# Optimization experiments

Measured on AMD Instinct MI355X. Metric: run time of the kernel, lower is better.

The kernel has to match this reference:

```python
import jax, jax.numpy as jnp
import numpy as np

N_NODES = 100000   # total atoms in the batched graph
N_EDGES = 1600000  # bonds (directed), avg degree 16
N_GRAPHS = 2000    # molecules in the batch
D_IN, D_H, D_OUT = 600, 300, 2  # 600 = embedding_dim(150) * 4


def setup_inputs() -> dict:
    key = jax.random.key(0)
    ks = jax.random.split(key, 8)
    node_feats = jax.random.normal(ks[0], (N_NODES, D_IN), dtype=jnp.float32)
    W1 = jax.random.normal(ks[1], (D_IN, D_H), dtype=jnp.float32) * (1.0 / np.sqrt(D_IN))
    b1 = jnp.zeros((D_H,), dtype=jnp.float32)
    W2 = jax.random.normal(ks[2], (D_H, D_H), dtype=jnp.float32) * (1.0 / np.sqrt(D_H))
    b2 = jnp.zeros((D_H,), dtype=jnp.float32)
    Wfc = jax.random.normal(ks[3], (D_H, D_OUT), dtype=jnp.float32) * (1.0 / np.sqrt(D_H))
    bfc = jnp.zeros((D_OUT,), dtype=jnp.float32)
    src = jax.random.randint(ks[4], (N_EDGES,), 0, N_NODES, dtype=jnp.int32).astype(jnp.int64)
    dst = jax.random.randint(ks[5], (N_EDGES,), 0, N_NODES, dtype=jnp.int32).astype(jnp.int64)
    graph_id = jnp.sort(jax.random.randint(ks[6], (N_NODES,), 0, N_GRAPHS, dtype=jnp.int32)).astype(jnp.int64)
    return {"node_feats": node_feats, "W1": W1, "b1": b1, "W2": W2, "b2": b2,
            "Wfc": Wfc, "bfc": bfc, "src": src, "dst": dst, "graph_id": graph_id}


def _gcn_layer(x, W, b, src, dst, inv_sqrt_out, inv_sqrt_in):
    # DGL GraphConv (norm='both'): h_i = d_i^{-1/2} * sum_{j->i} d_j^{-1/2} (x_j W) + b
    # weight applied before aggregation (in_feats >= out_feats path), math identical either way.
    h = x @ W                                  # [N, d_out]
    m = h * inv_sqrt_out[:, None]              # scale by src out-degree^{-1/2}
    agg = jax.ops.segment_sum(m[src], dst, num_segments=N_NODES)  # [N, d_out]
    return agg * inv_sqrt_in[:, None] + b


def reference(node_feats, W1, b1, W2, b2, Wfc, bfc, src, dst, graph_id):
    ones_e = jnp.ones((src.shape[0],), dtype=node_feats.dtype)
    deg_out = jax.ops.segment_sum(ones_e, src, num_segments=N_NODES)
    deg_in = jax.ops.segment_sum(ones_e, dst, num_segments=N_NODES)
    inv_sqrt_out = jnp.where(deg_out > 0, jax.lax.rsqrt(jnp.maximum(deg_out, 1.0)), 0.0)
    inv_sqrt_in = jnp.where(deg_in > 0, jax.lax.rsqrt(jnp.maximum(deg_in, 1.0)), 0.0)

    h = jax.nn.relu(_gcn_layer(node_feats, W1, b1, src, dst, inv_sqrt_out, inv_sqrt_in))
    h = jax.nn.relu(_gcn_layer(h, W2, b2, src, dst, inv_sqrt_out, inv_sqrt_in))
    p = jax.nn.softmax(h @ Wfc + bfc, axis=-1)  # [N, 2] per-node class probs

    # per-graph mean pooling (unbatch + mean over each graph's nodes)
    pooled_sum = jax.ops.segment_sum(p, graph_id, num_segments=N_GRAPHS)
    counts = jax.ops.segment_sum(jnp.ones((N_NODES,), dtype=p.dtype), graph_id, num_segments=N_GRAPHS)
    return pooled_sum / jnp.maximum(counts, 1.0)[:, None]  # [G, 2]
```

## Files before the change

kernel.cpp:

```cpp
#include <hip/hip_runtime.h>
#include <hip/hip_bf16.h>
#include <hip/hip_fp8.h>

#define N_NODES 100000
#define N_EDGES 1600000
#define N_GRAPHS 2000
#define D_IN 600
#define D_H 300
#define D_OUT 2

#define NPAD 320
#define K1PAD 640
#define K2PAD 320
#define MPAD 100096

typedef __bf16 bf16;
typedef __bf16 bf16x8 __attribute__((ext_vector_type(8)));
typedef float f32x4 __attribute__((ext_vector_type(4)));

__device__ __forceinline__ void gload16(const void* g, void* l) {
    __builtin_amdgcn_global_load_lds(
        (const __attribute__((address_space(1))) unsigned int*)g,
        (__attribute__((address_space(3))) unsigned int*)l, 16, 0, 0);
}

__device__ __forceinline__ float f8f(unsigned int b) {
    __hip_fp8_e4m3 t; t.__x = (__hip_fp8_storage_t)b; return (float)t;
}
__device__ __forceinline__ unsigned char ff8(float f) {
    __hip_fp8_e4m3 t(f); return (unsigned char)t.__x;
}

__global__ __launch_bounds__(256) void count_deg(const int* __restrict__ src,
                                                 const int* __restrict__ dst,
                                                 int* __restrict__ deg_out,
                                                 int* __restrict__ deg_in) {
    int e = blockIdx.x * blockDim.x + threadIdx.x;
    if (e < N_EDGES) {
        atomicAdd(&deg_out[src[e]], 1);
        atomicAdd(&deg_in[dst[e]], 1);
    }
}

__global__ __launch_bounds__(256) void block_sum(const int* __restrict__ deg_in,
                                                 int* __restrict__ bsum) {
    __shared__ int s[256];
    int i = blockIdx.x * 256 + threadIdx.x;
    s[threadIdx.x] = (i < N_NODES) ? deg_in[i] : 0;
    __syncthreads();
    for (int off = 128; off; off >>= 1) {
        if (threadIdx.x < off) s[threadIdx.x] += s[threadIdx.x + off];
        __syncthreads();
    }
    if (threadIdx.x == 0) bsum[blockIdx.x] = s[0];
}

__global__ void scan_serial(const int* __restrict__ bsum, int* __restrict__ boff, int nb) {
    if (threadIdx.x == 0 && blockIdx.x == 0) {
        int run = 0;
        for (int i = 0; i < nb; ++i) { boff[i] = run; run += bsum[i]; }
    }
}

__global__ __launch_bounds__(256) void node_offsets(const int* __restrict__ deg_in,
                                                    const int* __restrict__ deg_out,
                                                    const int* __restrict__ boff,
                                                    int* __restrict__ row_start,
                                                    int* __restrict__ cursor,
                                                    float* __restrict__ inv_in,
                                                    float* __restrict__ inv_out) {
    __shared__ int s[256];
    int i = blockIdx.x * 256 + threadIdx.x;
    int d = (i < N_NODES) ? deg_in[i] : 0;
    s[threadIdx.x] = d;
    __syncthreads();
    for (int off = 1; off < 256; off <<= 1) {
        int v = 0;
        if (threadIdx.x >= off) v = s[threadIdx.x - off];
        __syncthreads();
        if (threadIdx.x >= off) s[threadIdx.x] += v;
        __syncthreads();
    }
    if (i < N_NODES) {
        int excl = s[threadIdx.x] - d;
        int rs = boff[blockIdx.x] + excl;
        row_start[i] = rs;
        cursor[i] = rs;
        int di = deg_in[i];
        int dout = deg_out[i];
        inv_in[i]  = (di   > 0) ? rsqrtf((float)di)   : 0.0f;
        inv_out[i] = (dout > 0) ? rsqrtf((float)dout) : 0.0f;
    }
}

__global__ __launch_bounds__(256) void fill_csr(const int* __restrict__ src,
                                                const int* __restrict__ dst,
                                                int* __restrict__ cursor,
                                                int* __restrict__ adj) {
    int e = blockIdx.x * blockDim.x + threadIdx.x;
    if (e < N_EDGES) {
        int pos = atomicAdd(&cursor[dst[e]], 1);
        adj[pos] = src[e];
    }
}

__global__ __launch_bounds__(256) void conv_bt(const float* __restrict__ W, bf16* __restrict__ Bt,
                                               int K, int N, int Kpad) {
    int idx = blockIdx.x * 256 + threadIdx.x;
    int k = idx % Kpad;
    int n = idx / Kpad;
    if (n >= NPAD) return;
    bf16 v = (bf16)0.0f;
    if (k < K && n < N) v = (bf16)W[(size_t)k * N + n];
    Bt[(size_t)n * Kpad + k] = v;
}

__global__ __launch_bounds__(256) void prep_small(const float* __restrict__ b1,
                                                  const float* __restrict__ b2,
                                                  const float* __restrict__ Wfc,
                                                  float* __restrict__ b1p,
                                                  float* __restrict__ b2p,
                                                  float* __restrict__ wfcp) {
    int i = blockIdx.x * 256 + threadIdx.x;
    if (i < NPAD) {
        b1p[i] = (i < D_H) ? b1[i] : 0.f;
        b2p[i] = (i < D_H) ? b2[i] : 0.f;
    }
    if (i < NPAD * 2) {
        wfcp[i] = (i < D_H * 2) ? Wfc[i] : 0.f;
    }
}

__global__ __launch_bounds__(512) void mfma_gemm_f32A(const float* __restrict__ A,
                                                      const bf16* __restrict__ Bt,
                                                      const float* __restrict__ rowscale,
                                                      unsigned char* __restrict__ C8) {
    __shared__ bf16 As[128 * 64];
    __shared__ bf16 Bs[320 * 64];
    const int tid = threadIdx.x;
    const int lane = tid & 63;
    const int wid = tid >> 6;
    const int wr = wid >> 2;
    const int wc = wid & 3;
    const int blockRow = blockIdx.x * 128;
    const size_t rowBytesB = (size_t)K1PAD * 2;

    f32x4 acc[4][5] = {};

    const int nK = K1PAD >> 6;
    for (int t = 0; t < nK; ++t) {
        const size_t kByte = (size_t)t * 128;
#pragma unroll
        for (int c = 0; c < 2; ++c) {
            int o = c * 8192 + tid * 16;
            int row = o >> 7;
            int slot = (o >> 4) & 7;
            int gr = blockRow + row;
            int k = t * 64 + slot * 8;
            bf16x8 v = {};
            if (gr < N_NODES && k < D_IN) {
                const float* p = A + (size_t)gr * D_IN + k;
                float4 f0 = *(const float4*)p;
                float4 f1 = *(const float4*)(p + 4);
                v[0] = (bf16)f0.x; v[1] = (bf16)f0.y; v[2] = (bf16)f0.z; v[3] = (bf16)f0.w;
                v[4] = (bf16)f1.x; v[5] = (bf16)f1.y; v[6] = (bf16)f1.z; v[7] = (bf16)f1.w;
            }
            int waddr = row * 128 + ((slot ^ (row & 7)) << 4);
            *(bf16x8*)((char*)As + waddr) = v;
        }
#pragma unroll
        for (int c = 0; c < 5; ++c) {
            int o = c * 8192 + tid * 16;
            int row = o >> 7;
            int slot = (o >> 4) & 7;
            int srcs = slot ^ (row & 7);
            const char* g = (const char*)Bt + (size_t)row * rowBytesB + kByte + srcs * 16;
            gload16(g, (char*)Bs + o);
        }
        __syncthreads();
#pragma unroll
        for (int kk = 0; kk < 2; ++kk) {
            int slot = kk * 4 + (lane >> 4);
            bf16x8 af[4], bfr[5];
#pragma unroll
            for (int mi = 0; mi < 4; ++mi) {
                int row = wr * 64 + mi * 16 + (lane & 15);
                int addr = row * 128 + ((slot ^ (row & 7)) << 4);
                af[mi] = *(const bf16x8*)((const char*)As + addr);
            }
#pragma unroll
            for (int ni = 0; ni < 5; ++ni) {
                int row = wc * 80 + ni * 16 + (lane & 15);
                int addr = row * 128 + ((slot ^ (row & 7)) << 4);
                bfr[ni] = *(const bf16x8*)((const char*)Bs + addr);
            }
#pragma unroll
            for (int mi = 0; mi < 4; ++mi)
#pragma unroll
                for (int ni = 0; ni < 5; ++ni)
                    acc[mi][ni] = __builtin_amdgcn_mfma_f32_16x16x32_bf16(af[mi], bfr[ni], acc[mi][ni], 0, 0, 0);
        }
        __syncthreads();
    }
#pragma unroll
    for (int mi = 0; mi < 4; ++mi) {
#pragma unroll
        for (int i = 0; i < 4; ++i) {
            int gr = blockRow + wr * 64 + mi * 16 + ((lane >> 4) << 2) + i;
            if (gr >= N_NODES) continue;
            float sc = rowscale[gr];
#pragma unroll
            for (int ni = 0; ni < 5; ++ni) {
                int gc = wc * 80 + ni * 16 + (lane & 15);
                C8[(size_t)gr * NPAD + gc] = ff8(acc[mi][ni][i] * sc);
            }
        }
    }
}

__global__ __launch_bounds__(512) void mfma_gemm(const bf16* __restrict__ A,
                                                 const bf16* __restrict__ Bt,
                                                 const float* __restrict__ rowscale,
                                                 unsigned char* __restrict__ C8,
                                                 int M, int Kpad) {
    __shared__ bf16 As[128 * 64];
    __shared__ bf16 Bs[320 * 64];
    const int tid = threadIdx.x;
    const int lane = tid & 63;
    const int wid = tid >> 6;
    const int wr = wid >> 2;
    const int wc = wid & 3;
    const int blockRow = blockIdx.x * 128;
    const size_t rowBytes = (size_t)Kpad * 2;

    f32x4 acc[4][5] = {};

    const int nK = Kpad >> 6;
    for (int t = 0; t < nK; ++t) {
        const size_t kByte = (size_t)t * 128;
#pragma unroll
        for (int c = 0; c < 2; ++c) {
            int o = c * 8192 + tid * 16;
            int row = o >> 7;
            int slot = (o >> 4) & 7;
            int srcs = slot ^ (row & 7);
            const char* g = (const char*)A + (size_t)(blockRow + row) * rowBytes + kByte + srcs * 16;
            gload16(g, (char*)As + o);
        }
#pragma unroll
        for (int c = 0; c < 5; ++c) {
            int o = c * 8192 + tid * 16;
            int row = o >> 7;
            int slot = (o >> 4) & 7;
            int srcs = slot ^ (row & 7);
            const char* g = (const char*)Bt + (size_t)row * rowBytes + kByte + srcs * 16;
            gload16(g, (char*)Bs + o);
        }
        __syncthreads();
#pragma unroll
        for (int kk = 0; kk < 2; ++kk) {
            int slot = kk * 4 + (lane >> 4);
            bf16x8 af[4], bfr[5];
#pragma unroll
            for (int mi = 0; mi < 4; ++mi) {
                int row = wr * 64 + mi * 16 + (lane & 15);
                int addr = row * 128 + ((slot ^ (row & 7)) << 4);
                af[mi] = *(const bf16x8*)((const char*)As + addr);
            }
#pragma unroll
            for (int ni = 0; ni < 5; ++ni) {
                int row = wc * 80 + ni * 16 + (lane & 15);
                int addr = row * 128 + ((slot ^ (row & 7)) << 4);
                bfr[ni] = *(const bf16x8*)((const char*)Bs + addr);
            }
#pragma unroll
            for (int mi = 0; mi < 4; ++mi)
#pragma unroll
                for (int ni = 0; ni < 5; ++ni)
                    acc[mi][ni] = __builtin_amdgcn_mfma_f32_16x16x32_bf16(af[mi], bfr[ni], acc[mi][ni], 0, 0, 0);
        }
        __syncthreads();
    }
#pragma unroll
    for (int mi = 0; mi < 4; ++mi) {
#pragma unroll
        for (int i = 0; i < 4; ++i) {
            int gr = blockRow + wr * 64 + mi * 16 + ((lane >> 4) << 2) + i;
            if (gr >= M) continue;
            float sc = rowscale[gr];
#pragma unroll
            for (int ni = 0; ni < 5; ++ni) {
                int gc = wc * 80 + ni * 16 + (lane & 15);
                C8[(size_t)gr * NPAD + gc] = ff8(acc[mi][ni][i] * sc);
            }
        }
    }
}

__device__ __forceinline__ void gather_fp8(const unsigned char* __restrict__ m8,
                                           const int* __restrict__ adj,
                                           int s, int d, int lane, float acc[5]) {
    const int cb = lane * 4;
    const int c4 = 256 + lane;
    int e = 0;
    for (; e + 4 <= d; e += 4) {
        const unsigned char* r0 = m8 + (size_t)adj[s + e + 0] * NPAD;
        const unsigned char* r1 = m8 + (size_t)adj[s + e + 1] * NPAD;
        const unsigned char* r2 = m8 + (size_t)adj[s + e + 2] * NPAD;
        const unsigned char* r3 = m8 + (size_t)adj[s + e + 3] * NPAD;
        unsigned int u0 = *(const unsigned int*)(r0 + cb);
        unsigned int u1 = *(const unsigned int*)(r1 + cb);
        unsigned int u2 = *(const unsigned int*)(r2 + cb);
        unsigned int u3 = *(const unsigned int*)(r3 + cb);
        unsigned int b0 = r0[c4], b1 = r1[c4], b2 = r2[c4], b3 = r3[c4];
        acc[0] += (f8f(u0 & 0xff) + f8f(u1 & 0xff)) + (f8f(u2 & 0xff) + f8f(u3 & 0xff));
        acc[1] += (f8f((u0 >> 8) & 0xff) + f8f((u1 >> 8) & 0xff)) + (f8f((u2 >> 8) & 0xff) + f8f((u3 >> 8) & 0xff));
        acc[2] += (f8f((u0 >> 16) & 0xff) + f8f((u1 >> 16) & 0xff)) + (f8f((u2 >> 16) & 0xff) + f8f((u3 >> 16) & 0xff));
        acc[3] += (f8f(u0 >> 24) + f8f(u1 >> 24)) + (f8f(u2 >> 24) + f8f(u3 >> 24));
        acc[4] += (f8f(b0) + f8f(b1)) + (f8f(b2) + f8f(b3));
    }
    for (; e < d; ++e) {
        const unsigned char* r = m8 + (size_t)adj[s + e] * NPAD;
        unsigned int u = *(const unsigned int*)(r + cb);
        acc[0] += f8f(u & 0xff);
        acc[1] += f8f((u >> 8) & 0xff);
        acc[2] += f8f((u >> 16) & 0xff);
        acc[3] += f8f(u >> 24);
        acc[4] += f8f(r[c4]);
    }
}

__global__ __launch_bounds__(256) void aggregate_fp8(const unsigned char* __restrict__ m8,
                                                     const int* __restrict__ row_start,
                                                     const int* __restrict__ deg_in,
                                                     const int* __restrict__ adj,
                                                     const float* __restrict__ inv_in,
                                                     const float* __restrict__ biasp,
                                                     bf16* __restrict__ h) {
    int node = (int)((blockIdx.x * (size_t)blockDim.x + threadIdx.x) >> 6);
    int lane = threadIdx.x & 63;
    if (node >= N_NODES) return;
    int s = row_start[node];
    int d = deg_in[node];
    float acc[5] = {};
    gather_fp8(m8, adj, s, d, lane, acc);
    float sc = inv_in[node];
    int cA = lane * 4;
    int c4 = 256 + lane;
    float4 bq = *(const float4*)(biasp + cA);
    bf16* out = h + (size_t)node * NPAD;
    __bf16 o4[4];
    o4[0] = (bf16)fmaxf(acc[0] * sc + bq.x, 0.f);
    o4[1] = (bf16)fmaxf(acc[1] * sc + bq.y, 0.f);
    o4[2] = (bf16)fmaxf(acc[2] * sc + bq.z, 0.f);
    o4[3] = (bf16)fmaxf(acc[3] * sc + bq.w, 0.f);
    *(float2*)(out + cA) = *(float2*)o4;
    out[c4] = (bf16)fmaxf(acc[4] * sc + biasp[c4], 0.f);
}

__global__ __launch_bounds__(256) void agg2_fc_pool(const unsigned char* __restrict__ m8,
                                                    const int* __restrict__ row_start,
                                                    const int* __restrict__ deg_in,
                                                    const int* __restrict__ adj,
                                                    const float* __restrict__ inv_in,
                                                    const float* __restrict__ biasp,
                                                    const float* __restrict__ wfcp,
                                                    const float* __restrict__ bfc,
                                                    const int* __restrict__ gid,
                                                    float* __restrict__ pooled,
                                                    int* __restrict__ gcount) {
    int node = (int)((blockIdx.x * (size_t)blockDim.x + threadIdx.x) >> 6);
    int lane = threadIdx.x & 63;
    if (node >= N_NODES) return;
    int s = row_start[node];
    int d = deg_in[node];
    float acc[5] = {};
    gather_fp8(m8, adj, s, d, lane, acc);
    float sc = inv_in[node];
    int cA = lane * 4;
    int c4 = 256 + lane;
    float4 bq = *(const float4*)(biasp + cA);
    float h0 = fmaxf(acc[0] * sc + bq.x, 0.f);
    float h1 = fmaxf(acc[1] * sc + bq.y, 0.f);
    float h2 = fmaxf(acc[2] * sc + bq.z, 0.f);
    float h3 = fmaxf(acc[3] * sc + bq.w, 0.f);
    float h4 = fmaxf(acc[4] * sc + biasp[c4], 0.f);
    float4 wA0 = *(const float4*)(wfcp + cA * 2);
    float4 wA1 = *(const float4*)(wfcp + cA * 2 + 4);
    float z0 = h0 * wA0.x + h1 * wA0.z + h2 * wA1.x + h3 * wA1.z;
    float z1 = h0 * wA0.y + h1 * wA0.w + h2 * wA1.y + h3 * wA1.w;
    z0 += h4 * wfcp[c4 * 2];
    z1 += h4 * wfcp[c4 * 2 + 1];
    for (int off = 32; off; off >>= 1) {
        z0 += __shfl_down(z0, off);
        z1 += __shfl_down(z1, off);
    }
    if (lane == 0) {
        float s0 = z0 + bfc[0], s1 = z1 + bfc[1];
        float mx = fmaxf(s0, s1);
        float e0 = __expf(s0 - mx), e1 = __expf(s1 - mx);
        float inv = 1.f / (e0 + e1);
        int g = gid[node];
        atomicAdd(&pooled[g * 2 + 0], e0 * inv);
        atomicAdd(&pooled[g * 2 + 1], e1 * inv);
        atomicAdd(&gcount[g], 1);
    }
}

__global__ __launch_bounds__(256) void finalize(const float* __restrict__ pooled,
                                                const int* __restrict__ gcount,
                                                float* __restrict__ out) {
    int i = blockIdx.x * blockDim.x + threadIdx.x;
    if (i < N_GRAPHS * 2) {
        int g = i >> 1;
        float c = (float)max(gcount[g], 1);
        out[i] = pooled[i] / c;
    }
}

extern "C" void kernel_launch(void* const* d_in, const int* in_sizes, int n_in,
                              void* d_out, int out_size, void* d_ws, size_t ws_size,
                              hipStream_t stream) {
    const float* x   = (const float*)d_in[0];
    const float* W1  = (const float*)d_in[1];
    const float* b1  = (const float*)d_in[2];
    const float* W2  = (const float*)d_in[3];
    const float* b2  = (const float*)d_in[4];
    const float* Wfc = (const float*)d_in[5];
    const float* bfc = (const float*)d_in[6];
    const int* src   = (const int*)d_in[7];
    const int* dst   = (const int*)d_in[8];
    const int* gid   = (const int*)d_in[9];

    char* ws = (char*)d_ws;
    size_t off = 0;
    auto alloc = [&](size_t bytes) -> void* {
        void* p = ws + off;
        off = (off + bytes + 255) & ~(size_t)255;
        return p;
    };
    bf16* h_bf            = (bf16*)alloc((size_t)MPAD * NPAD * 2);
    unsigned char* m8     = (unsigned char*)alloc((size_t)N_NODES * NPAD);
    bf16* B1t    = (bf16*)alloc((size_t)NPAD * K1PAD * 2);
    bf16* B2t    = (bf16*)alloc((size_t)NPAD * K2PAD * 2);
    int*   adj      = (int*)alloc((size_t)N_EDGES * 4);
    int*   row_st   = (int*)alloc((size_t)N_NODES * 4);
    int*   cursor   = (int*)alloc((size_t)N_NODES * 4);
    int*   deg_in   = (int*)alloc((size_t)N_NODES * 4);
    int*   deg_out  = (int*)alloc((size_t)N_NODES * 4);
    float* inv_in   = (float*)alloc((size_t)N_NODES * 4);
    float* inv_out  = (float*)alloc((size_t)N_NODES * 4);
    const int NB = (N_NODES + 255) / 256;
    int*   bsum     = (int*)alloc((size_t)NB * 4);
    int*   boff     = (int*)alloc((size_t)NB * 4);
    float* pooled   = (float*)alloc((size_t)N_GRAPHS * 2 * 4);
    int*   gcount   = (int*)alloc((size_t)N_GRAPHS * 4);
    float* b1p      = (float*)alloc((size_t)NPAD * 4);
    float* b2p      = (float*)alloc((size_t)NPAD * 4);
    float* wfcp     = (float*)alloc((size_t)NPAD * 2 * 4);

    hipMemsetAsync(deg_in, 0, (size_t)N_NODES * 4, stream);
    hipMemsetAsync(deg_out, 0, (size_t)N_NODES * 4, stream);
    hipMemsetAsync(pooled, 0, (size_t)N_GRAPHS * 2 * 4, stream);
    hipMemsetAsync(gcount, 0, (size_t)N_GRAPHS * 4, stream);

    count_deg<<<(N_EDGES + 255) / 256, 256, 0, stream>>>(src, dst, deg_out, deg_in);
    block_sum<<<NB, 256, 0, stream>>>(deg_in, bsum);
    scan_serial<<<1, 64, 0, stream>>>(bsum, boff, NB);
    node_offsets<<<NB, 256, 0, stream>>>(deg_in, deg_out, boff, row_st, cursor, inv_in, inv_out);
    fill_csr<<<(N_EDGES + 255) / 256, 256, 0, stream>>>(src, dst, cursor, adj);

    conv_bt<<<(NPAD * K1PAD + 255) / 256, 256, 0, stream>>>(W1, B1t, D_IN, D_H, K1PAD);
    conv_bt<<<(NPAD * K2PAD + 255) / 256, 256, 0, stream>>>(W2, B2t, D_H, D_H, K2PAD);
    prep_small<<<3, 256, 0, stream>>>(b1, b2, Wfc, b1p, b2p, wfcp);

    mfma_gemm_f32A<<<MPAD / 128, 512, 0, stream>>>(x, B1t, inv_out, m8);
    aggregate_fp8<<<(N_NODES * 64 + 255) / 256, 256, 0, stream>>>(m8, row_st, deg_in, adj, inv_in, b1p, h_bf);
    mfma_gemm<<<MPAD / 128, 512, 0, stream>>>(h_bf, B2t, inv_out, m8, N_NODES, K2PAD);
    agg2_fc_pool<<<(N_NODES * 64 + 255) / 256, 256, 0, stream>>>(m8, row_st, deg_in, adj, inv_in, b2p,
                                                                 wfcp, bfc, gid, pooled, gcount);
    finalize<<<(N_GRAPHS * 2 + 255) / 256, 256, 0, stream>>>(pooled, gcount, (float*)d_out);
}
```

Baseline: 705.9 us.

## Prefetch next GEMM K-tile into registers while computing current tile

Both GEMM kernels are merged into one templated kernel that loads the next K-tile of A and B into registers while the MFMAs of the current tile run, then writes them to LDS after a barrier. This replaces the direct global-to-LDS loads and the synchronous per-tile load-then-compute pattern, aiming to hide global memory latency. It also precomputes the swizzled offsets and makes the K loop count a compile-time constant. The cost is more registers per thread, which may lower occupancy, and an extra pass of LDS writes through VGPRs.

```diff
diff --git a/kernel.cpp b/kernel.cpp
--- a/kernel.cpp
+++ b/kernel.cpp
@@ -17,12 +17,6 @@
 typedef __bf16 bf16;
 typedef __bf16 bf16x8 __attribute__((ext_vector_type(8)));
 typedef float f32x4 __attribute__((ext_vector_type(4)));
-
-__device__ __forceinline__ void gload16(const void* g, void* l) {
-    __builtin_amdgcn_global_load_lds(
-        (const __attribute__((address_space(1))) unsigned int*)g,
-        (__attribute__((address_space(3))) unsigned int*)l, 16, 0, 0);
-}
 
 __device__ __forceinline__ float f8f(unsigned int b) {
     __hip_fp8_e4m3 t; t.__x = (__hip_fp8_storage_t)b; return (float)t;
@@ -131,10 +125,13 @@
     }
 }
 
-__global__ __launch_bounds__(512) void mfma_gemm_f32A(const float* __restrict__ A,
-                                                      const bf16* __restrict__ Bt,
-                                                      const float* __restrict__ rowscale,
-                                                      unsigned char* __restrict__ C8) {
+template<int NK, bool AF32>
+__global__ __launch_bounds__(512) void gemm_rs(const float* __restrict__ Af,
+                                               const bf16* __restrict__ Ab,
+                                               const bf16* __restrict__ Bt,
+                                               const float* __restrict__ rowscale,
+                                               unsigned char* __restrict__ C8,
+                                               int M) {
     __shared__ bf16 As[128 * 64];
     __shared__ bf16 Bs[320 * 64];
     const int tid = threadIdx.x;
@@ -143,152 +140,113 @@
     const int wr = wid >> 2;
     const int wc = wid & 3;
     const int blockRow = blockIdx.x * 128;
-    const size_t rowBytesB = (size_t)K1PAD * 2;
+    const int Kpad = NK * 64;
+    const size_t rowBytes = (size_t)Kpad * 2;
 
     f32x4 acc[4][5] = {};
 
-    const int nK = K1PAD >> 6;
-    for (int t = 0; t < nK; ++t) {
-        const size_t kByte = (size_t)t * 128;
-#pragma unroll
+    int aO[2], aRow[2], aKs[2];
+    #pragma unroll
+    for (int c = 0; c < 2; ++c) {
+        int o = c * 8192 + tid * 16;
+        int row = o >> 7;
+        int slot = (o >> 4) & 7;
+        aO[c] = o; aRow[c] = row; aKs[c] = (slot ^ (row & 7)) * 8;
+    }
+    int bO[5], bRow[5], bKs[5];
+    #pragma unroll
+    for (int c = 0; c < 5; ++c) {
+        int o = c * 8192 + tid * 16;
+        int row = o >> 7;
+        int slot = (o >> 4) & 7;
+        bO[c] = o; bRow[c] = row; bKs[c] = (slot ^ (row & 7)) * 8;
+    }
+
+    float4 fA[2][2];
+    bf16x8 sA[2];
+    bf16x8 sB[5];
+
+    auto loadTile = [&](int t) {
+        #pragma unroll
         for (int c = 0; c < 2; ++c) {
-            int o = c * 8192 + tid * 16;
-            int row = o >> 7;
-            int slot = (o >> 4) & 7;
-            int gr = blockRow + row;
-            int k = t * 64 + slot * 8;
-            bf16x8 v = {};
-            if (gr < N_NODES && k < D_IN) {
-                const float* p = A + (size_t)gr * D_IN + k;
-                float4 f0 = *(const float4*)p;
-                float4 f1 = *(const float4*)(p + 4);
-                v[0] = (bf16)f0.x; v[1] = (bf16)f0.y; v[2] = (bf16)f0.z; v[3] = (bf16)f0.w;
-                v[4] = (bf16)f1.x; v[5] = (bf16)f1.y; v[6] = (bf16)f1.z; v[7] = (bf16)f1.w;
+            if (AF32) {
+                int gr = blockRow + aRow[c];
+                int k = t * 64 + aKs[c];
+                if (gr < N_NODES && k < D_IN) {
+                    const float* p = Af + (size_t)gr * D_IN + k;
+                    fA[c][0] = *(const float4*)p;
+                    fA[c][1] = *(const float4*)(p + 4);
+                } else {
+                    fA[c][0] = make_float4(0.f, 0.f, 0.f, 0.f);
+                    fA[c][1] = make_float4(0.f, 0.f, 0.f, 0.f);
+                }
+            } else {
+                const char* g = (const char*)Ab + (size_t)(blockRow + aRow[c]) * rowBytes
+                                + (size_t)t * 128 + aKs[c] * 2;
+                sA[c] = *(const bf16x8*)g;
             }
-            int waddr = row * 128 + ((slot ^ (row & 7)) << 4);
-            *(bf16x8*)((char*)As + waddr) = v;
         }
-#pragma unroll
+        #pragma unroll
         for (int c = 0; c < 5; ++c) {
-            int o = c * 8192 + tid * 16;
-            int row = o >> 7;
-            int slot = (o >> 4) & 7;
-            int srcs = slot ^ (row & 7);
-            const char* g = (const char*)Bt + (size_t)row * rowBytesB + kByte + srcs * 16;
-            gload16(g, (char*)Bs + o);
+            const char* g = (const char*)Bt + (size_t)bRow[c] * rowBytes
+                            + (size_t)t * 128 + bKs[c] * 2;
+            sB[c] = *(const bf16x8*)g;
         }
+    };
+
+    loadTile(0);
+
+    for (int t = 0; t < NK; ++t) {
         __syncthreads();
-#pragma unroll
+        #pragma unroll
+        for (int c = 0; c < 2; ++c) {
+            bf16x8 v;
+            if (AF32) {
+                v[0] = (bf16)fA[c][0].x; v[1] = (bf16)fA[c][0].y;
+                v[2] = (bf16)fA[c][0].z; v[3] = (bf16)fA[c][0].w;
+                v[4] = (bf16)fA[c][1].x; v[5] = (bf16)fA[c][1].y;
+                v[6] = (bf16)fA[c][1].z; v[7] = (bf16)fA[c][1].w;
+            } else {
+                v = sA[c];
+            }
+            *(bf16x8*)((char*)As + aO[c]) = v;
+        }
+        #pragma unroll
+        for (int c = 0; c < 5; ++c)
+            *(bf16x8*)((char*)Bs + bO[c]) = sB[c];
+        __syncthreads();
+        if (t + 1 < NK) loadTile(t + 1);
+        #pragma unroll
         for (int kk = 0; kk < 2; ++kk) {
             int slot = kk * 4 + (lane >> 4);
             bf16x8 af[4], bfr[5];
-#pragma unroll
+            #pragma unroll
             for (int mi = 0; mi < 4; ++mi) {
                 int row = wr * 64 + mi * 16 + (lane & 15);
                 int addr = row * 128 + ((slot ^ (row & 7)) << 4);
                 af[mi] = *(const bf16x8*)((const char*)As + addr);
             }
-#pragma unroll
+            #pragma unroll
             for (int ni = 0; ni < 5; ++ni) {
                 int row = wc * 80 + ni * 16 + (lane & 15);
                 int addr = row * 128 + ((slot ^ (row & 7)) << 4);
                 bfr[ni] = *(const bf16x8*)((const char*)Bs + addr);
             }
-#pragma unroll
+            #pragma unroll
             for (int mi = 0; mi < 4; ++mi)
-#pragma unroll
+                #pragma unroll
                 for (int ni = 0; ni < 5; ++ni)
                     acc[mi][ni] = __builtin_amdgcn_mfma_f32_16x16x32_bf16(af[mi], bfr[ni], acc[mi][ni], 0, 0, 0);
         }
-        __syncthreads();
-    }
-#pragma unroll
+    }
+    #pragma unroll
     for (int mi = 0; mi < 4; ++mi) {
-#pragma unroll
-        for (int i = 0; i < 4; ++i) {
-            int gr = blockRow + wr * 64 + mi * 16 + ((lane >> 4) << 2) + i;
-            if (gr >= N_NODES) continue;
-            float sc = rowscale[gr];
-#pragma unroll
-            for (int ni = 0; ni < 5; ++ni) {
-                int gc = wc * 80 + ni * 16 + (lane & 15);
-                C8[(size_t)gr * NPAD + gc] = ff8(acc[mi][ni][i] * sc);
-            }
-        }
-    }
-}
-
-__global__ __launch_bounds__(512) void mfma_gemm(const bf16* __restrict__ A,
-                                                 const bf16* __restrict__ Bt,
-                                                 const float* __restrict__ rowscale,
-                                                 unsigned char* __restrict__ C8,
-                                                 int M, int Kpad) {
-    __shared__ bf16 As[128 * 64];
-    __shared__ bf16 Bs[320 * 64];
-    const int tid = threadIdx.x;
-    const int lane = tid & 63;
-    const int wid = tid >> 6;
-    const int wr = wid >> 2;
-    const int wc = wid & 3;
-    const int blockRow = blockIdx.x * 128;
-    const size_t rowBytes = (size_t)Kpad * 2;
-
-    f32x4 acc[4][5] = {};
-
-    const int nK = Kpad >> 6;
-    for (int t = 0; t < nK; ++t) {
-        const size_t kByte = (size_t)t * 128;
-#pragma unroll
-        for (int c = 0; c < 2; ++c) {
-            int o = c * 8192 + tid * 16;
-            int row = o >> 7;
-            int slot = (o >> 4) & 7;
-            int srcs = slot ^ (row & 7);
-            const char* g = (const char*)A + (size_t)(blockRow + row) * rowBytes + kByte + srcs * 16;
-            gload16(g, (char*)As + o);
-        }
-#pragma unroll
-        for (int c = 0; c < 5; ++c) {
-            int o = c * 8192 + tid * 16;
-            int row = o >> 7;
-            int slot = (o >> 4) & 7;
-            int srcs = slot ^ (row & 7);
-            const char* g = (const char*)Bt + (size_t)row * rowBytes + kByte + srcs * 16;
-            gload16(g, (char*)Bs + o);
-        }
-        __syncthreads();
-#pragma unroll
-        for (int kk = 0; kk < 2; ++kk) {
-            int slot = kk * 4 + (lane >> 4);
-            bf16x8 af[4], bfr[5];
-#pragma unroll
-            for (int mi = 0; mi < 4; ++mi) {
-                int row = wr * 64 + mi * 16 + (lane & 15);
-                int addr = row * 128 + ((slot ^ (row & 7)) << 4);
-                af[mi] = *(const bf16x8*)((const char*)As + addr);
-            }
-#pragma unroll
-            for (int ni = 0; ni < 5; ++ni) {
-                int row = wc * 80 + ni * 16 + (lane & 15);
-                int addr = row * 128 + ((slot ^ (row & 7)) << 4);
-                bfr[ni] = *(const bf16x8*)((const char*)Bs + addr);
-            }
-#pragma unroll
-            for (int mi = 0; mi < 4; ++mi)
-#pragma unroll
-                for (int ni = 0; ni < 5; ++ni)
-                    acc[mi][ni] = __builtin_amdgcn_mfma_f32_16x16x32_bf16(af[mi], bfr[ni], acc[mi][ni], 0, 0, 0);
-        }
-        __syncthreads();
-    }
-#pragma unroll
-    for (int mi = 0; mi < 4; ++mi) {
-#pragma unroll
+        #pragma unroll
         for (int i = 0; i < 4; ++i) {
             int gr = blockRow + wr * 64 + mi * 16 + ((lane >> 4) << 2) + i;
             if (gr >= M) continue;
             float sc = rowscale[gr];
-#pragma unroll
+            #pragma unroll
             for (int ni = 0; ni < 5; ++ni) {
                 int gc = wc * 80 + ni * 16 + (lane & 15);
                 C8[(size_t)gr * NPAD + gc] = ff8(acc[mi][ni][i] * sc);
@@ -474,9 +432,9 @@
     conv_bt<<<(NPAD * K2PAD + 255) / 256, 256, 0, stream>>>(W2, B2t, D_H, D_H, K2PAD);
     prep_small<<<3, 256, 0, stream>>>(b1, b2, Wfc, b1p, b2p, wfcp);
 
-    mfma_gemm_f32A<<<MPAD / 128, 512, 0, stream>>>(x, B1t, inv_out, m8);
+    gemm_rs<10, true><<<MPAD / 128, 512, 0, stream>>>(x, nullptr, B1t, inv_out, m8, N_NODES);
     aggregate_fp8<<<(N_NODES * 64 + 255) / 256, 256, 0, stream>>>(m8, row_st, deg_in, adj, inv_in, b1p, h_bf);
-    mfma_gemm<<<MPAD / 128, 512, 0, stream>>>(h_bf, B2t, inv_out, m8, N_NODES, K2PAD);
+    gemm_rs<5, false><<<MPAD / 128, 512, 0, stream>>>(nullptr, h_bf, B2t, inv_out, m8, N_NODES);
     agg2_fc_pool<<<(N_NODES * 64 + 255) / 256, 256, 0, stream>>>(m8, row_st, deg_in, adj, inv_in, b2p,
                                                                  wfcp, bfc, gid, pooled, gcount);
     finalize<<<(N_GRAPHS * 2 + 255) / 256, 256, 0, stream>>>(pooled, gcount, (float*)d_out);
```

New measurement: 684.7 us. -3.0%, faster.
